# Kernel tuning notes

Measured on AMD Instinct MI355X. Metric: run time of the kernel, lower is better.

The kernel has to match this reference:

```python
import jax, jax.numpy as jnp
from jax import lax
import numpy as np

RADIUS = 2.0
K = 32          # max_neighbors
KNN = 3         # knn_num for FP interpolation
DEPTH = 3
NH = 16         # nhidden
NIN = 16
NOUT = 2
N = 16384
BOX = 32.0


def sqdist(a, b):
    # a: [M,3], b: [N,3] -> [M,N] squared distances (no [M,N,3] intermediate)
    d2 = (jnp.sum(a * a, -1)[:, None] + jnp.sum(b * b, -1)[None, :]
          - 2.0 * a @ b.T)
    return jnp.maximum(d2, 0.0)


def fps(pos, m):
    # farthest point sampling, deterministic start at index 0 (eval mode)
    n = pos.shape[0]
    def step(carry, _):
        mind, last = carry
        d = jnp.sum((pos - pos[last]) ** 2, axis=-1)
        mind = jnp.minimum(mind, d)
        nxt = jnp.argmax(mind).astype(jnp.int32)
        return (mind, nxt), nxt
    init = (jnp.full((n,), jnp.inf, dtype=pos.dtype), jnp.array(0, jnp.int32))
    _, rest = lax.scan(step, init, None, length=m - 1)
    return jnp.concatenate([jnp.zeros((1,), jnp.int32), rest])


def radius_group(pos_tgt, pos_src, r, k):
    # up-to-k neighbors of each target within radius r (nearest-first)
    d2 = sqdist(pos_tgt, pos_src)                      # [M,N]
    neg = jnp.where(d2 <= r * r, -d2, -jnp.inf)
    vals, cols = lax.top_k(neg, k)                     # [M,K]
    valid = jnp.isfinite(vals)
    return cols, valid


def knn_interpolate(x_c, pos_c, pos_f, k):
    d2 = sqdist(pos_f, pos_c)                          # [Nf, Nc]
    negv, nn = lax.top_k(-d2, k)                       # k nearest coarse pts
    w = 1.0 / jnp.maximum(-negv, 1e-16)
    w = w / jnp.sum(w, -1, keepdims=True)
    return jnp.sum(x_c[nn] * w[..., None], axis=1)     # [Nf, C]


def mlp2(h, W0, b0, W1, b1, act_last=True):
    h = jax.nn.relu(h @ W0 + b0)
    h = h @ W1 + b1
    return jax.nn.relu(h) if act_last else h


def setup_inputs() -> dict:
    key = jax.random.key(0)
    ks = jax.random.split(key, 24)
    s = 0.2
    dim_sa = NH + 3   # 19: PointConv concat(x_j, rel_pos)
    dim_fp = NH + NH  # 32: FP concat(interp, skip)
    return {
        "x": jax.random.normal(ks[0], (N, NIN), jnp.float32),
        "pos": jax.random.uniform(ks[1], (N, 3), jnp.float32) * BOX,
        "batch": jnp.zeros((N,), jnp.int32),
        "lin_in_W0": jax.random.normal(ks[2], (NIN, NH)) * s,
        "lin_in_b0": jnp.zeros((NH,), jnp.float32),
        "lin_in_W1": jax.random.normal(ks[3], (NH, NH)) * s,
        "lin_in_b1": jnp.zeros((NH,), jnp.float32),
        "sa_W0": jax.random.normal(ks[4], (DEPTH, dim_sa, dim_sa)) * s,
        "sa_b0": jnp.zeros((DEPTH, dim_sa), jnp.float32),
        "sa_W1": jax.random.normal(ks[5], (DEPTH, dim_sa, NH)) * s,
        "sa_b1": jnp.zeros((DEPTH, NH), jnp.float32),
        "fp_W0": jax.random.normal(ks[6], (DEPTH, dim_fp, dim_fp)) * s,
        "fp_b0": jnp.zeros((DEPTH, dim_fp), jnp.float32),
        "fp_W1": jax.random.normal(ks[7], (DEPTH, dim_fp, NH)) * s,
        "fp_b1": jnp.zeros((DEPTH, NH), jnp.float32),
        "lo_W0": jax.random.normal(ks[8], (NH, NH)) * s,
        "lo_b0": jnp.zeros((NH,), jnp.float32),
        "lo_W1": jax.random.normal(ks[9], (NH, NOUT)) * s,
        "lo_b1": jnp.zeros((NOUT,), jnp.float32),
    }


def reference(x, pos, batch,
              lin_in_W0, lin_in_b0, lin_in_W1, lin_in_b1,
              sa_W0, sa_b0, sa_W1, sa_b1,
              fp_W0, fp_b0, fp_W1, fp_b1,
              lo_W0, lo_b0, lo_W1, lo_b1):
    # lin_in MLP
    h = mlp2(x, lin_in_W0, lin_in_b0, lin_in_W1, lin_in_b1)
    sa = [(h, pos)]
    # SA (downsampling) path
    for i in range(DEPTH):
        xi, pi = sa[i]
        m = pi.shape[0] // 2                      # ratio = 0.5
        idx = fps(pi, m)
        pt = pi[idx]                              # sampled centers [M,3]
        cols, valid = radius_group(pt, pi, RADIUS, K)   # [M,K]
        xj = xi[cols]                             # [M,K,NH]
        rel = pi[cols] - pt[:, None, :]           # [M,K,3]
        msg = jnp.concatenate([xj, rel], -1)      # [M,K,19]
        msg = mlp2(msg, sa_W0[i], sa_b0[i], sa_W1[i], sa_b1[i])
        msg = jnp.where(valid[..., None], msg, -1e30)
        xn = jnp.max(msg, axis=1)                 # max aggregation (PointConv)
        sa.append((xn, pt))
    # FP (upsampling) path
    xf, pf = sa[DEPTH]
    for i in range(DEPTH - 1, -1, -1):
        xs, ps = sa[i]
        xi = knn_interpolate(xf, pf, ps, KNN)
        hcat = jnp.concatenate([xi, xs], -1)      # [Nf, 32]
        xf = mlp2(hcat, fp_W0[i], fp_b0[i], fp_W1[i], fp_b1[i])
        pf = ps
    # lin_out: relu then linear (act=['relu', None])
    return mlp2(xf, lo_W0, lo_b0, lo_W1, lo_b1, act_last=False)
```

## Files before the change

kernel.cpp:

```cpp
#include <hip/hip_runtime.h>
#include <stdint.h>


#define DEV static __device__ __forceinline__

DEV float fadd_(float a, float b){ return __fadd_rn(a,b); }
DEV float fsub_(float a, float b){ return __fsub_rn(a,b); }
DEV float fmul_(float a, float b){ return __fmul_rn(a,b); }
DEV float fdiv_(float a, float b){ return __fdiv_rn(a,b); }

DEV float dot3(float ax,float ay,float az,float bx,float by,float bz){
  return fmaf(az,bz, fmaf(ay,by, __fmul_rn(ax,bx)));
}
DEV float sqd(float na, float nb, float d){
  float t = __fadd_rn(na, nb);
  float u = __fmul_rn(2.0f, d);
  return fmaxf(__fsub_rn(t, u), 0.0f);
}

DEV float bbd2(float sx,float sy,float sz,
               float lx,float ly,float lz,float hx,float hy,float hz){
  float dx = fmaxf(fmaxf(fsub_(lx,sx), fsub_(sx,hx)), 0.0f);
  float dy = fmaxf(fmaxf(fsub_(ly,sy), fsub_(sy,hy)), 0.0f);
  float dz = fmaxf(fmaxf(fsub_(lz,sz), fsub_(sz,hz)), 0.0f);
  return fadd_(fadd_(fmul_(dx,dx),fmul_(dy,dy)),fmul_(dz,dz));
}

#define DPP0(src, ctrl, rm, bc) \
  __builtin_amdgcn_update_dpp(0, (int)(src), (ctrl), (rm), 0xf, (bc))

#define DPP64(dst, src, ctrl, rm, bc) { \
  uint32_t lo_ = (uint32_t)DPP0((uint32_t)(src), ctrl, rm, bc); \
  uint32_t hi_ = (uint32_t)DPP0((uint32_t)((src)>>32), ctrl, rm, bc); \
  (dst) = (((unsigned long long)hi_)<<32) | lo_; }

#define MERGE2(A1, A2, ctrl, rm, bc) { \
  unsigned long long b1_, b2_, mn_, mx_; \
  DPP64(b1_, A1, ctrl, rm, bc); \
  DPP64(b2_, A2, ctrl, rm, bc); \
  mn_ = (A1) < b1_ ? (A1) : b1_; \
  mx_ = (A2) > b2_ ? (A2) : b2_; \
  (A1) = (A1) > b1_ ? (A1) : b1_; \
  (A2) = mn_ > mx_ ? mn_ : mx_; }

DEV unsigned long long rdlane64(unsigned long long v, int l){
  uint32_t lo=(uint32_t)__builtin_amdgcn_readlane((int)(uint32_t)v, l);
  uint32_t hi=(uint32_t)__builtin_amdgcn_readlane((int)(uint32_t)(v>>32), l);
  return (((unsigned long long)hi)<<32)|lo;
}

DEV void wtop2(unsigned long long &A1, unsigned long long &A2){
  MERGE2(A1,A2,0x111,0xf,true)
  MERGE2(A1,A2,0x112,0xf,true)
  MERGE2(A1,A2,0x114,0xf,true)
  MERGE2(A1,A2,0x118,0xf,true)
  MERGE2(A1,A2,0x142,0xa,false)
  MERGE2(A1,A2,0x143,0xc,false)
  A1 = rdlane64(A1,63); A2 = rdlane64(A2,63);
}
DEV void htop2(unsigned long long &A1, unsigned long long &A2){
  MERGE2(A1,A2,0x111,0xf,true)
  MERGE2(A1,A2,0x112,0xf,true)
  MERGE2(A1,A2,0x114,0xf,true)
  MERGE2(A1,A2,0x118,0xf,true)
  MERGE2(A1,A2,0x142,0xa,false)
  A1 = rdlane64(A1,31); A2 = rdlane64(A2,31);
}

__global__ __launch_bounds__(256) void k_prep(
    const float* __restrict__ x, const float* __restrict__ pos,
    const float* __restrict__ W0, const float* __restrict__ b0,
    const float* __restrict__ W1, const float* __restrict__ b1,
    float4* __restrict__ pos4, float* __restrict__ h_out, int n)
{
  __shared__ float sW0[256], sb0[16], sW1[256], sb1[16];
  int tid = threadIdx.x;
  sW0[tid] = W0[tid];
  sW1[tid] = W1[tid];
  if (tid < 16){ sb0[tid] = b0[tid]; sb1[tid] = b1[tid]; }
  __syncthreads();
  int p = blockIdx.x*256 + tid;
  if (p >= n) return;

  float px = pos[3*p], py = pos[3*p+1], pz = pos[3*p+2];
  float nrm = fadd_(fadd_(fmul_(px,px), fmul_(py,py)), fmul_(pz,pz));
  pos4[p] = make_float4(px,py,pz,nrm);

  const float4* xr = (const float4*)(x + (size_t)p*16);
  float4 v0 = xr[0], v1 = xr[1], v2 = xr[2], v3 = xr[3];
  float xin[16] = {v0.x,v0.y,v0.z,v0.w, v1.x,v1.y,v1.z,v1.w,
                   v2.x,v2.y,v2.z,v2.w, v3.x,v3.y,v3.z,v3.w};
  float h1[16];
  #pragma unroll
  for (int o=0;o<16;o++){
    float acc = fmul_(xin[0], sW0[o]);
    #pragma unroll
    for (int k=1;k<16;k++) acc = fmaf(xin[k], sW0[k*16+o], acc);
    h1[o] = fmaxf(fadd_(acc, sb0[o]), 0.0f);
  }
  float h2[16];
  #pragma unroll
  for (int o=0;o<16;o++){
    float acc = fmul_(h1[0], sW1[o]);
    #pragma unroll
    for (int k=1;k<16;k++) acc = fmaf(h1[k], sW1[k*16+o], acc);
    h2[o] = fmaxf(fadd_(acc, sb1[o]), 0.0f);
  }
  float4* hw = (float4*)(h_out + (size_t)p*16);
  hw[0] = make_float4(h2[0], h2[1], h2[2], h2[3]);
  hw[1] = make_float4(h2[4], h2[5], h2[6], h2[7]);
  hw[2] = make_float4(h2[8], h2[9], h2[10],h2[11]);
  hw[3] = make_float4(h2[12],h2[13],h2[14],h2[15]);
}

DEV uint32_t expand4(uint32_t v){
  return (v&1u) | ((v&2u)<<2) | ((v&4u)<<4) | ((v&8u)<<6);
}
DEV int cellc(float v){
  int c = (int)(v*0.5f);
  return c < 0 ? 0 : (c > 15 ? 15 : c);
}
DEV uint32_t mkey(float4 p){
  return expand4((uint32_t)cellc(p.x))
       | (expand4((uint32_t)cellc(p.y))<<1)
       | (expand4((uint32_t)cellc(p.z))<<2);
}

__global__ __launch_bounds__(1024) void k_sort(
  const float4* __restrict__ nat, float4* __restrict__ srt,
  int* __restrict__ rank0, int n)
{
  __shared__ uint32_t hist[4096];
  __shared__ uint32_t gsum[1024];
  int tid = threadIdx.x;
  for (int i=tid;i<4096;i+=1024) hist[i]=0u;
  __syncthreads();
  for (int i=tid;i<n;i+=1024){
    float4 p = nat[i];
    atomicAdd(&hist[mkey(p)], 1u);
  }
  __syncthreads();
  uint32_t h0=hist[4*tid],h1=hist[4*tid+1],h2=hist[4*tid+2],h3=hist[4*tid+3];
  gsum[tid] = h0+h1+h2+h3;
  __syncthreads();
  for (int off=1; off<1024; off<<=1){
    uint32_t v = gsum[tid];
    uint32_t a = (tid>=off)? gsum[tid-off] : 0u;
    __syncthreads();
    gsum[tid] = v + a;
    __syncthreads();
  }
  uint32_t excl = (tid>0)? gsum[tid-1] : 0u;
  hist[4*tid]   = excl;
  hist[4*tid+1] = excl + h0;
  hist[4*tid+2] = excl + h0 + h1;
  hist[4*tid+3] = excl + h0 + h1 + h2;
  __syncthreads();
  for (int i=tid;i<n;i+=1024){
    float4 p = nat[i];
    uint32_t r = atomicAdd(&hist[mkey(p)], 1u);
    srt[r] = make_float4(p.x, p.y, p.z, __uint_as_float((uint32_t)i));
    if (i==0) *rank0 = (int)r;
  }
}

template<int P>
__global__ __attribute__((amdgpu_waves_per_eu(4,4)))
__launch_bounds__(1024) void k_fps5(
    const float4* __restrict__ sp4,
    const int* __restrict__ rank0p,
    float4* __restrict__ samp,
    int m)
{
  __shared__ float smind[P*1024];
  __shared__ uint32_t xch[2][32*5];
  const int t = threadIdx.x;
  const int lane = t & 63;
  const int w = t >> 6;

  float px[P], py[P], pz[P];
  uint32_t klo[P];
  float blox,bloy,bloz,bhix,bhiy,bhiz;
  #pragma unroll
  for (int k=0;k<P;k++){
    float4 p = sp4[t*P+k];
    px[k]=p.x; py[k]=p.y; pz[k]=p.z;
    uint32_t nat = __float_as_uint(p.w);
    klo[k] = ((0x3FFFu - nat)<<16) | (uint32_t)(t*P+k);
    smind[k*1024+t] = __builtin_inff();
    if (k==0){ blox=bhix=p.x; bloy=bhiy=p.y; bloz=bhiz=p.z; }
    else {
      blox=fminf(blox,p.x); bhix=fmaxf(bhix,p.x);
      bloy=fminf(bloy,p.y); bhiy=fmaxf(bhiy,p.y);
      bloz=fminf(bloz,p.z); bhiz=fmaxf(bhiz,p.z);
    }
  }

  float c1x,c1y,c1z, c2x=0.f,c2y=0.f,c2z=0.f;
  {
    int r0 = *rank0p;
    float4 s0 = sp4[r0];
    c1x=s0.x; c1y=s0.y; c1z=s0.z;
    if (t==0){
      float nr = fadd_(fadd_(fmul_(s0.x,s0.x),fmul_(s0.y,s0.y)),fmul_(s0.z,s0.z));
      samp[0] = make_float4(s0.x,s0.y,s0.z,nr);
    }
  }
  __syncthreads();

  unsigned long long tc1 = ((unsigned long long)0x7f800000u)<<32, tc2 = 0ull;
  bool own1 = false, own2 = false;
  uint32_t c1lo=0,c1hi=0, c2lo=0,c2hi=0;
  float o1x=0,o1y=0,o1z=0, o2x=0,o2y=0,o2z=0;

  int u2 = 0, sel = 1, round = 0;

  while (true){
    bool updp;
    {
      float cv = __uint_as_float((uint32_t)(tc1>>32));
      float dm = bbd2(c1x,c1y,c1z, blox,bloy,bloz,bhix,bhiy,bhiz);
      if (u2){
        float dd = bbd2(c2x,c2y,c2z, blox,bloy,bloz,bhix,bhiy,bhiz);
        dm = fminf(dm, dd);
      }
      updp = (fmul_(dm, 0.99999f) < cv);
    }
    if (__ballot(updp) != 0ull){
      if (updp){
        tc1 = 0ull; tc2 = 0ull;
        #pragma unroll
        for (int k=0;k<P;k++){
          float dx=fsub_(px[k],c1x), dy=fsub_(py[k],c1y), dz=fsub_(pz[k],c1z);
          float da = fadd_(fadd_(fmul_(dx,dx),fmul_(dy,dy)),fmul_(dz,dz));
          float nm = fminf(smind[k*1024+t], da);
          if (u2){
            float ex=fsub_(px[k],c2x), ey=fsub_(py[k],c2y), ez=fsub_(pz[k],c2z);
            float db = fadd_(fadd_(fmul_(ex,ex),fmul_(ey,ey)),fmul_(ez,ez));
            nm = fminf(nm, db);
          }
          smind[k*1024+t] = nm;
          unsigned long long key =
            (((unsigned long long)__float_as_uint(nm))<<32) | klo[k];
          bool g1 = key > tc1;
          unsigned long long nt2 = g1 ? tc1 : (key > tc2 ? key : tc2);
          tc1 = g1 ? key : tc1;
          tc2 = nt2;
        }
      }
      unsigned long long a1 = tc1, a2 = tc2;
      wtop2(a1, a2);
      own1 = (tc1 == a1);
      own2 = (tc1 == a2) || (tc2 == a2);
      int kk1 = (int)(a1 & (unsigned long long)(P-1));
      int kk2 = (int)(a2 & (unsigned long long)(P-1));
      float sx1=px[0], sy1=py[0], sz1=pz[0];
      float sx2=px[0], sy2=py[0], sz2=pz[0];
      #pragma unroll
      for (int j=1;j<P;j++){
        bool e1=(j==kk1), e2=(j==kk2);
        sx1=e1?px[j]:sx1; sy1=e1?py[j]:sy1; sz1=e1?pz[j]:sz1;
        sx2=e2?px[j]:sx2; sy2=e2?py[j]:sy2; sz2=e2?pz[j]:sz2;
      }
      c1lo=(uint32_t)a1; c1hi=(uint32_t)(a1>>32); o1x=sx1; o1y=sy1; o1z=sz1;
      c2lo=(uint32_t)a2; c2hi=(uint32_t)(a2>>32); o2x=sx2; o2y=sy2; o2z=sz2;
    }
    int par = round & 1;
    if (own1){
      int b = (w*2)*5;
      xch[par][b]=c1lo; xch[par][b+1]=c1hi;
      xch[par][b+2]=__float_as_uint(o1x);
      xch[par][b+3]=__float_as_uint(o1y);
      xch[par][b+4]=__float_as_uint(o1z);
    }
    if (own2){
      int b = (w*2+1)*5;
      xch[par][b]=c2lo; xch[par][b+1]=c2hi;
      xch[par][b+2]=__float_as_uint(o2x);
      xch[par][b+3]=__float_as_uint(o2y);
      xch[par][b+4]=__float_as_uint(o2z);
    }
    __syncthreads();
    unsigned long long cnd = 0ull;
    if (lane < 32){
      uint32_t lo = xch[par][lane*5], hi = xch[par][lane*5+1];
      cnd = (((unsigned long long)hi)<<32) | lo;
    }
    unsigned long long a1 = cnd, a2 = 0ull;
    htop2(a1, a2);
    unsigned long long b1 = __ballot(lane<32 && cnd==a1);
    unsigned long long b2 = __ballot(lane<32 && cnd==a2);
    int s1 = __ffsll(b1)-1;
    int s2 = __ffsll(b2)-1;
    float p1x=__uint_as_float(xch[par][s1*5+2]);
    float p1y=__uint_as_float(xch[par][s1*5+3]);
    float p1z=__uint_as_float(xch[par][s1*5+4]);
    float p2x=__uint_as_float(xch[par][s2*5+2]);
    float p2y=__uint_as_float(xch[par][s2*5+3]);
    float p2z=__uint_as_float(xch[par][s2*5+4]);
    float v2 = __uint_as_float((uint32_t)(a2>>32));
    float qx=fsub_(p2x,p1x), qy=fsub_(p2y,p1y), qz=fsub_(p2z,p1z);
    float q  = fadd_(fadd_(fmul_(qx,qx),fmul_(qy,qy)),fmul_(qz,qz));
    bool acc2 = (sel+1 < m) && (q >= v2);
    if (t==0){
      float nr = fadd_(fadd_(fmul_(p1x,p1x),fmul_(p1y,p1y)),fmul_(p1z,p1z));
      samp[sel] = make_float4(p1x,p1y,p1z,nr);
    }
    if (acc2 && t==1){
      float nr = fadd_(fadd_(fmul_(p2x,p2x),fmul_(p2y,p2y)),fmul_(p2z,p2z));
      samp[sel+1] = make_float4(p2x,p2y,p2z,nr);
    }
    sel += acc2 ? 2 : 1;
    round++;
    if (sel >= m) break;
    c1x=p1x; c1y=p1y; c1z=p1z;
    u2 = acc2 ? 1 : 0;
    if (acc2){ c2x=p2x; c2y=p2y; c2z=p2z; }
  }
}

#define SA_CAP 96

__global__ __launch_bounds__(256) void k_sa(
  const float4* __restrict__ spos, int n_src,
  const float4* __restrict__ tpos,
  const float*  __restrict__ F,
  const float* __restrict__ W0, const float* __restrict__ b0,
  const float* __restrict__ W1, const float* __restrict__ b1,
  float* __restrict__ Fout)
{
  __shared__ float sW0[361], sb0[19], sW1[304], sb1[16];
  __shared__ int   nidx[4][SA_CAP];
  __shared__ float nd2[4][SA_CAP];
  int tid = threadIdx.x;
  for (int i=tid;i<361;i+=256) sW0[i]=W0[i];
  for (int i=tid;i<304;i+=256) sW1[i]=W1[i];
  if (tid<19) sb0[tid]=b0[tid];
  if (tid<16) sb1[tid]=b1[tid];
  __syncthreads();

  int wv = tid >> 6, lane = tid & 63;
  int tg = blockIdx.x*4 + wv;
  float4 tp = tpos[tg];

  int cnt = 0;
  for (int base=0; base<n_src; base+=64){
    int j = base + lane;
    float4 sp = spos[j];
    float d2 = sqd(tp.w, sp.w, dot3(tp.x,tp.y,tp.z, sp.x,sp.y,sp.z));
    bool in = (d2 <= 4.0f);
    unsigned long long mk = __ballot(in);
    int pos = cnt + __popcll(mk & ((1ull<<lane)-1ull));
    if (in && pos < SA_CAP){ nidx[wv][pos]=j; nd2[wv][pos]=d2; }
    cnt += __popcll(mk);
  }
  if (cnt > SA_CAP) cnt = SA_CAP;

  if (cnt > 32){
    uint64_t tk0=0, tk1=0;
    for (int r=0;r<32;r++){
      float bvv = 3.5e38f; int bii = 0x7fffffff; int be = 0;
      for (int e=0;e<cnt;e++){
        bool done = (e<64) ? ((tk0>>e)&1ull) : ((tk1>>(e-64))&1ull);
        if (done) continue;
        float dv = nd2[wv][e]; int di = nidx[wv][e];
        if (dv < bvv || (dv == bvv && di < bii)){ bvv=dv; bii=di; be=e; }
      }
      if (be < 64) tk0 |= (1ull<<be); else tk1 |= (1ull<<(be-64));
    }
    int myi = 0; float myd = 0.0f;
    if (lane < 32){
      int seen = 0, sel = -1;
      for (int e=0;e<cnt && sel<0;e++){
        bool s = (e<64) ? ((tk0>>e)&1ull) : ((tk1>>(e-64))&1ull);
        if (s){ if (seen == lane) sel = e; seen++; }
      }
      myi = nidx[wv][sel]; myd = nd2[wv][sel];
    }
    __builtin_amdgcn_wave_barrier();
    if (lane < 32){ nidx[wv][lane]=myi; nd2[wv][lane]=myd; }
    __builtin_amdgcn_wave_barrier();
    cnt = 32;
  }

  float in19[19];
  #pragma unroll
  for (int k=0;k<19;k++) in19[k] = 0.0f;
  if (lane < cnt){
    int j = nidx[wv][lane];
    const float4* fr = (const float4*)(F + (size_t)j*16);
    float4 a=fr[0], b=fr[1], c=fr[2], d=fr[3];
    in19[0]=a.x; in19[1]=a.y; in19[2]=a.z; in19[3]=a.w;
    in19[4]=b.x; in19[5]=b.y; in19[6]=b.z; in19[7]=b.w;
    in19[8]=c.x; in19[9]=c.y; in19[10]=c.z; in19[11]=c.w;
    in19[12]=d.x; in19[13]=d.y; in19[14]=d.z; in19[15]=d.w;
    float4 sp = spos[j];
    in19[16]=fsub_(sp.x,tp.x); in19[17]=fsub_(sp.y,tp.y); in19[18]=fsub_(sp.z,tp.z);
  }
  float h[19];
  #pragma unroll
  for (int o=0;o<19;o++){
    float acc = fmul_(in19[0], sW0[o]);
    #pragma unroll
    for (int k=1;k<19;k++) acc = fmaf(in19[k], sW0[k*19+o], acc);
    h[o] = fmaxf(fadd_(acc, sb0[o]), 0.0f);
  }
  float outv[16];
  #pragma unroll
  for (int o=0;o<16;o++){
    float acc = fmul_(h[0], sW1[o]);
    #pragma unroll
    for (int k=1;k<19;k++) acc = fmaf(h[k], sW1[k*16+o], acc);
    float v = fmaxf(fadd_(acc, sb1[o]), 0.0f);
    outv[o] = (lane < cnt) ? v : -1e30f;
  }
  #pragma unroll
  for (int o=0;o<16;o++){
    float v = outv[o];
    #pragma unroll
    for (int s=1;s<64;s<<=1) v = fmaxf(v, __shfl_xor(v, s));
    outv[o] = v;
  }
  if (lane == 0){
    float4* dst = (float4*)(Fout + (size_t)tg*16);
    dst[0] = make_float4(outv[0], outv[1], outv[2], outv[3]);
    dst[1] = make_float4(outv[4], outv[5], outv[6], outv[7]);
    dst[2] = make_float4(outv[8], outv[9], outv[10],outv[11]);
    dst[3] = make_float4(outv[12],outv[13],outv[14],outv[15]);
  }
}

__global__ __launch_bounds__(256) void k_fp(
  const float4* __restrict__ fpos,
  const float4* __restrict__ cpos, int n_coarse,
  const float* __restrict__ Fc, const float* __restrict__ Fs,
  const float* __restrict__ W0, const float* __restrict__ b0,
  const float* __restrict__ W1, const float* __restrict__ b1,
  const float* __restrict__ loW0, const float* __restrict__ lob0,
  const float* __restrict__ loW1, const float* __restrict__ lob1,
  float* __restrict__ outp, int final_)
{
  __shared__ float sW0[1024], sb0[32], sW1[512], sb1[16];
  __shared__ float sLW0[256], sLb0[16], sLW1[32], sLb1[2];
  int tid = threadIdx.x;
  for (int i=tid;i<1024;i+=256) sW0[i]=W0[i];
  for (int i=tid;i<512;i+=256)  sW1[i]=W1[i];
  if (tid<32) sb0[tid]=b0[tid];
  if (tid<16) sb1[tid]=b1[tid];
  if (final_){
    sLW0[tid & 255] = loW0[tid & 255];
    if (tid<16) sLb0[tid]=lob0[tid];
    if (tid<32) sLW1[tid]=loW1[tid];
    if (tid<2)  sLb1[tid]=lob1[tid];
  }
  __syncthreads();

  int wv = tid >> 6, lane = tid & 63;
  int f = blockIdx.x*4 + wv;
  float4 fp = fpos[f];

  float c0v=3.5e38f, c1v=3.5e38f, c2v=3.5e38f;
  int   c0i=0x7fffffff, c1i=0x7fffffff, c2i=0x7fffffff;
  for (int j=lane; j<n_coarse; j+=64){
    float4 cp = cpos[j];
    float d2 = sqd(fp.w, cp.w, dot3(fp.x,fp.y,fp.z, cp.x,cp.y,cp.z));
    if (d2 < c2v || (d2 == c2v && j < c2i)){
      bool a0 = (d2 < c0v) || (d2 == c0v && j < c0i);
      bool a1 = (d2 < c1v) || (d2 == c1v && j < c1i);
      c2v = a1 ? c1v : d2;               c2i = a1 ? c1i : j;
      c1v = a0 ? c0v : (a1 ? d2 : c1v);  c1i = a0 ? c0i : (a1 ? j : c1i);
      c0v = a0 ? d2 : c0v;               c0i = a0 ? j  : c0i;
    }
  }
  float nnd[3]; int nni[3];
  #pragma unroll
  for (int r=0;r<3;r++){
    float v = c0v; int idx = c0i;
    #pragma unroll
    for (int s=1;s<64;s<<=1){
      float ov = __shfl_xor(v, s);
      int   oi = __shfl_xor(idx, s);
      bool tk = (ov < v) || (ov == v && oi < idx);
      v = tk ? ov : v; idx = tk ? oi : idx;
    }
    nnd[r] = v; nni[r] = idx;
    if (c0v == v && c0i == idx){
      c0v=c1v; c0i=c1i; c1v=c2v; c1i=c2i; c2v=3.5e38f; c2i=0x7fffffff;
    }
  }
  float w0 = fdiv_(1.0f, fmaxf(nnd[0], 1e-16f));
  float w1 = fdiv_(1.0f, fmaxf(nnd[1], 1e-16f));
  float w2 = fdiv_(1.0f, fmaxf(nnd[2], 1e-16f));
  float ws = fadd_(fadd_(w0,w1),w2);
  w0 = fdiv_(w0,ws); w1 = fdiv_(w1,ws); w2 = fdiv_(w2,ws);

  float hv = 0.0f;
  if (lane < 16){
    int c = lane;
    float x0 = Fc[(size_t)nni[0]*16 + c];
    float x1 = Fc[(size_t)nni[1]*16 + c];
    float x2 = Fc[(size_t)nni[2]*16 + c];
    hv = fadd_(fadd_(fmul_(w0,x0), fmul_(w1,x1)), fmul_(w2,x2));
  } else if (lane < 32){
    hv = Fs[(size_t)f*16 + (lane-16)];
  }
  int o1 = lane & 31;
  float acc = fmul_(__shfl(hv, 0), sW0[o1]);
  #pragma unroll
  for (int k=1;k<32;k++) acc = fmaf(__shfl(hv, k), sW0[k*32+o1], acc);
  float g1 = fmaxf(fadd_(acc, sb0[o1]), 0.0f);
  int o2 = lane & 15;
  float a2 = fmul_(__shfl(g1, 0), sW1[o2]);
  #pragma unroll
  for (int k=1;k<32;k++) a2 = fmaf(__shfl(g1, k), sW1[k*16+o2], a2);
  float g2 = fmaxf(fadd_(a2, sb1[o2]), 0.0f);

  if (!final_){
    if (lane < 16) outp[(size_t)f*16 + lane] = g2;
  } else {
    float a3 = fmul_(__shfl(g2, 0), sLW0[o2]);
    #pragma unroll
    for (int k=1;k<16;k++) a3 = fmaf(__shfl(g2, k), sLW0[k*16+o2], a3);
    float q = fmaxf(fadd_(a3, sLb0[o2]), 0.0f);
    int o3 = lane & 1;
    float a4 = fmul_(__shfl(q, 0), sLW1[o3]);
    #pragma unroll
    for (int k=1;k<16;k++) a4 = fmaf(__shfl(q, k), sLW1[k*2+o3], a4);
    a4 = fadd_(a4, sLb1[o3]);
    if (lane < 2) outp[(size_t)f*2 + lane] = a4;
  }
}

extern "C" void kernel_launch(void* const* d_in, const int* in_sizes, int n_in,
                              void* d_out, int out_size, void* d_ws, size_t ws_size,
                              hipStream_t stream) {
  (void)in_sizes; (void)n_in; (void)out_size; (void)ws_size;
  const float* x     = (const float*)d_in[0];
  const float* pos   = (const float*)d_in[1];
  const float* liW0  = (const float*)d_in[3];
  const float* lib0  = (const float*)d_in[4];
  const float* liW1  = (const float*)d_in[5];
  const float* lib1  = (const float*)d_in[6];
  const float* saW0  = (const float*)d_in[7];
  const float* sab0  = (const float*)d_in[8];
  const float* saW1  = (const float*)d_in[9];
  const float* sab1  = (const float*)d_in[10];
  const float* fpW0  = (const float*)d_in[11];
  const float* fpb0  = (const float*)d_in[12];
  const float* fpW1  = (const float*)d_in[13];
  const float* fpb1  = (const float*)d_in[14];
  const float* loW0  = (const float*)d_in[15];
  const float* lob0  = (const float*)d_in[16];
  const float* loW1  = (const float*)d_in[17];
  const float* lob1  = (const float*)d_in[18];
  float* out = (float*)d_out;

  char* ws = (char*)d_ws;
  size_t off = 0;
  auto alloc = [&](size_t bytes)->void* {
    void* p = ws + off;
    off += (bytes + 255) & ~(size_t)255;
    return p;
  };
  float4* P0 = (float4*)alloc(16384u*16);
  float4* P1 = (float4*)alloc(8192u*16);
  float4* P2 = (float4*)alloc(4096u*16);
  float4* P3 = (float4*)alloc(2048u*16);
  float*  F0 = (float*)alloc(16384u*16*4);
  float*  F1 = (float*)alloc(8192u*16*4);
  float*  F2 = (float*)alloc(4096u*16*4);
  float*  F3 = (float*)alloc(2048u*16*4);
  float*  G2 = (float*)alloc(4096u*16*4);
  float*  G1 = (float*)alloc(8192u*16*4);
  float4* S0 = (float4*)alloc(16384u*16);
  float4* S1 = (float4*)alloc(8192u*16);
  float4* S2 = (float4*)alloc(4096u*16);
  int*    R0 = (int*)alloc(256);

  k_prep<<<64,256,0,stream>>>(x,pos, liW0,lib0,liW1,lib1, P0,F0, 16384);

  k_sort<<<1,1024,0,stream>>>(P0, S0, R0+0, 16384);
  k_fps5<16><<<1,1024,0,stream>>>(S0, R0+0, P1, 8192);
  k_sa<<<2048,256,0,stream>>>(P0,16384, P1, F0, saW0,      sab0,    saW1,      sab1,    F1);
  k_sort<<<1,1024,0,stream>>>(P1, S1, R0+1, 8192);
  k_fps5<8><<<1,1024,0,stream>>>(S1, R0+1, P2, 4096);
  k_sa<<<1024,256,0,stream>>>(P1, 8192, P2, F1, saW0+361,  sab0+19, saW1+304,  sab1+16, F2);
  k_sort<<<1,1024,0,stream>>>(P2, S2, R0+2, 4096);
  k_fps5<4><<<1,1024,0,stream>>>(S2, R0+2, P3, 2048);
  k_sa<<< 512,256,0,stream>>>(P2, 4096, P3, F2, saW0+722,  sab0+38, saW1+608,  sab1+32, F3);

  k_fp<<<1024,256,0,stream>>>(P2, P3,2048, F3, F2,
      fpW0+2048, fpb0+64, fpW1+1024, fpb1+32,
      loW0,lob0,loW1,lob1, G2, 0);
  k_fp<<<2048,256,0,stream>>>(P1, P2,4096, G2, F1,
      fpW0+1024, fpb0+32, fpW1+512,  fpb1+16,
      loW0,lob0,loW1,lob1, G1, 0);
  k_fp<<<4096,256,0,stream>>>(P0, P1,8192, G1, F0,
      fpW0,      fpb0,    fpW1,      fpb1,
      loW0,lob0,loW1,lob1, out, 1);
}
```

Baseline: 20.61 ms.

## Extend FPS speculative selection from top-2 to top-4 candidates per round

The farthest-point-sampling kernel now keeps a per-thread and per-wave top-4 instead of top-2, and accepts up to four new samples per round when each candidate is at least as far from the earlier accepted candidates as its own min-distance. This cuts the number of serial block-wide rounds and barriers in the single-block FPS loop. Candidate coordinates are now re-read from global memory by sorted index instead of being passed through shared memory. In exchange each round does more DPP merge work and more distance updates per point.

```diff
diff --git a/kernel.cpp b/kernel.cpp
--- a/kernel.cpp
+++ b/kernel.cpp
@@ -16,6 +16,14 @@
   float t = __fadd_rn(na, nb);
   float u = __fmul_rn(2.0f, d);
   return fmaxf(__fsub_rn(t, u), 0.0f);
+}
+
+DEV float d2f_(float ax,float ay,float az,float bx,float by,float bz){
+  float dx=fsub_(ax,bx), dy=fsub_(ay,by), dz=fsub_(az,bz);
+  return fadd_(fadd_(fmul_(dx,dx),fmul_(dy,dy)),fmul_(dz,dz));
+}
+DEV float nrm3_(float x,float y,float z){
+  return fadd_(fadd_(fmul_(x,x),fmul_(y,y)),fmul_(z,z));
 }
 
 DEV float bbd2(float sx,float sy,float sz,
@@ -26,6 +34,10 @@
   return fadd_(fadd_(fmul_(dx,dx),fmul_(dy,dy)),fmul_(dz,dz));
 }
 
+DEV float rfl_f(float v){
+  return __int_as_float(__builtin_amdgcn_readfirstlane(__float_as_int(v)));
+}
+
 #define DPP0(src, ctrl, rm, bc) \
   __builtin_amdgcn_update_dpp(0, (int)(src), (ctrl), (rm), 0xf, (bc))
 
@@ -34,14 +46,21 @@
   uint32_t hi_ = (uint32_t)DPP0((uint32_t)((src)>>32), ctrl, rm, bc); \
   (dst) = (((unsigned long long)hi_)<<32) | lo_; }
 
-#define MERGE2(A1, A2, ctrl, rm, bc) { \
-  unsigned long long b1_, b2_, mn_, mx_; \
+#define MERGE4(A1,A2,A3,A4, ctrl, rm, bc) { \
+  unsigned long long b1_,b2_,b3_,b4_, m1_,m2_,m3_,m4_, t_; \
   DPP64(b1_, A1, ctrl, rm, bc); \
   DPP64(b2_, A2, ctrl, rm, bc); \
-  mn_ = (A1) < b1_ ? (A1) : b1_; \
-  mx_ = (A2) > b2_ ? (A2) : b2_; \
-  (A1) = (A1) > b1_ ? (A1) : b1_; \
-  (A2) = mn_ > mx_ ? mn_ : mx_; }
+  DPP64(b3_, A3, ctrl, rm, bc); \
+  DPP64(b4_, A4, ctrl, rm, bc); \
+  m1_ = (A1) > b4_ ? (A1) : b4_; \
+  m2_ = (A2) > b3_ ? (A2) : b3_; \
+  m3_ = (A3) > b2_ ? (A3) : b2_; \
+  m4_ = (A4) > b1_ ? (A4) : b1_; \
+  t_ = m1_ < m3_ ? m1_ : m3_;  m1_ = m1_ > m3_ ? m1_ : m3_;  m3_ = t_; \
+  t_ = m2_ < m4_ ? m2_ : m4_;  m2_ = m2_ > m4_ ? m2_ : m4_;  m4_ = t_; \
+  t_ = m1_ < m2_ ? m1_ : m2_;  m1_ = m1_ > m2_ ? m1_ : m2_;  m2_ = t_; \
+  t_ = m3_ < m4_ ? m3_ : m4_;  m3_ = m3_ > m4_ ? m3_ : m4_;  m4_ = t_; \
+  (A1)=m1_; (A2)=m2_; (A3)=m3_; (A4)=m4_; }
 
 DEV unsigned long long rdlane64(unsigned long long v, int l){
   uint32_t lo=(uint32_t)__builtin_amdgcn_readlane((int)(uint32_t)v, l);
@@ -49,22 +68,16 @@
   return (((unsigned long long)hi)<<32)|lo;
 }
 
-DEV void wtop2(unsigned long long &A1, unsigned long long &A2){
-  MERGE2(A1,A2,0x111,0xf,true)
-  MERGE2(A1,A2,0x112,0xf,true)
-  MERGE2(A1,A2,0x114,0xf,true)
-  MERGE2(A1,A2,0x118,0xf,true)
-  MERGE2(A1,A2,0x142,0xa,false)
-  MERGE2(A1,A2,0x143,0xc,false)
+DEV void wtop4(unsigned long long &A1, unsigned long long &A2,
+               unsigned long long &A3, unsigned long long &A4){
+  MERGE4(A1,A2,A3,A4,0x111,0xf,true)
+  MERGE4(A1,A2,A3,A4,0x112,0xf,true)
+  MERGE4(A1,A2,A3,A4,0x114,0xf,true)
+  MERGE4(A1,A2,A3,A4,0x118,0xf,true)
+  MERGE4(A1,A2,A3,A4,0x142,0xa,false)
+  MERGE4(A1,A2,A3,A4,0x143,0xc,false)
   A1 = rdlane64(A1,63); A2 = rdlane64(A2,63);
-}
-DEV void htop2(unsigned long long &A1, unsigned long long &A2){
-  MERGE2(A1,A2,0x111,0xf,true)
-  MERGE2(A1,A2,0x112,0xf,true)
-  MERGE2(A1,A2,0x114,0xf,true)
-  MERGE2(A1,A2,0x118,0xf,true)
-  MERGE2(A1,A2,0x142,0xa,false)
-  A1 = rdlane64(A1,31); A2 = rdlane64(A2,31);
+  A3 = rdlane64(A3,63); A4 = rdlane64(A4,63);
 }
 
 __global__ __launch_bounds__(256) void k_prep(
@@ -166,14 +179,14 @@
 
 template<int P>
 __global__ __attribute__((amdgpu_waves_per_eu(4,4)))
-__launch_bounds__(1024) void k_fps5(
+__launch_bounds__(1024) void k_fps6(
     const float4* __restrict__ sp4,
     const int* __restrict__ rank0p,
     float4* __restrict__ samp,
     int m)
 {
   __shared__ float smind[P*1024];
-  __shared__ uint32_t xch[2][32*5];
+  __shared__ unsigned long long xch[2][64];
   const int t = threadIdx.x;
   const int lane = t & 63;
   const int w = t >> 6;
@@ -196,126 +209,98 @@
     }
   }
 
-  float c1x,c1y,c1z, c2x=0.f,c2y=0.f,c2z=0.f;
+  float c0x,c0y,c0z;
+  float c1x=0.f,c1y=0.f,c1z=0.f, c2x=0.f,c2y=0.f,c2z=0.f;
+  float c3x=0.f,c3y=0.f,c3z=0.f;
   {
     int r0 = *rank0p;
     float4 s0 = sp4[r0];
-    c1x=s0.x; c1y=s0.y; c1z=s0.z;
+    c0x=s0.x; c0y=s0.y; c0z=s0.z;
     if (t==0){
-      float nr = fadd_(fadd_(fmul_(s0.x,s0.x),fmul_(s0.y,s0.y)),fmul_(s0.z,s0.z));
-      samp[0] = make_float4(s0.x,s0.y,s0.z,nr);
-    }
-  }
-  __syncthreads();
-
-  unsigned long long tc1 = ((unsigned long long)0x7f800000u)<<32, tc2 = 0ull;
-  bool own1 = false, own2 = false;
-  uint32_t c1lo=0,c1hi=0, c2lo=0,c2hi=0;
-  float o1x=0,o1y=0,o1z=0, o2x=0,o2y=0,o2z=0;
-
-  int u2 = 0, sel = 1, round = 0;
+      samp[0] = make_float4(s0.x,s0.y,s0.z, nrm3_(s0.x,s0.y,s0.z));
+    }
+  }
+  __syncthreads();
+
+  unsigned long long tc1 = ((unsigned long long)0x7f800000u)<<32;
+  unsigned long long tc2 = 0ull, tc3 = 0ull, tc4 = 0ull;
+  unsigned long long a1=0ull,a2=0ull,a3=0ull,a4=0ull;
+
+  int u = 1, sel = 1, round = 0;
 
   while (true){
     bool updp;
     {
       float cv = __uint_as_float((uint32_t)(tc1>>32));
-      float dm = bbd2(c1x,c1y,c1z, blox,bloy,bloz,bhix,bhiy,bhiz);
-      if (u2){
-        float dd = bbd2(c2x,c2y,c2z, blox,bloy,bloz,bhix,bhiy,bhiz);
-        dm = fminf(dm, dd);
-      }
+      float dm = bbd2(c0x,c0y,c0z, blox,bloy,bloz,bhix,bhiy,bhiz);
+      if (u>1) dm = fminf(dm, bbd2(c1x,c1y,c1z, blox,bloy,bloz,bhix,bhiy,bhiz));
+      if (u>2) dm = fminf(dm, bbd2(c2x,c2y,c2z, blox,bloy,bloz,bhix,bhiy,bhiz));
+      if (u>3) dm = fminf(dm, bbd2(c3x,c3y,c3z, blox,bloy,bloz,bhix,bhiy,bhiz));
       updp = (fmul_(dm, 0.99999f) < cv);
     }
     if (__ballot(updp) != 0ull){
       if (updp){
-        tc1 = 0ull; tc2 = 0ull;
+        tc1 = 0ull; tc2 = 0ull; tc3 = 0ull; tc4 = 0ull;
         #pragma unroll
         for (int k=0;k<P;k++){
-          float dx=fsub_(px[k],c1x), dy=fsub_(py[k],c1y), dz=fsub_(pz[k],c1z);
-          float da = fadd_(fadd_(fmul_(dx,dx),fmul_(dy,dy)),fmul_(dz,dz));
-          float nm = fminf(smind[k*1024+t], da);
-          if (u2){
-            float ex=fsub_(px[k],c2x), ey=fsub_(py[k],c2y), ez=fsub_(pz[k],c2z);
-            float db = fadd_(fadd_(fmul_(ex,ex),fmul_(ey,ey)),fmul_(ez,ez));
-            nm = fminf(nm, db);
-          }
+          float nm = smind[k*1024+t];
+          nm = fminf(nm, d2f_(px[k],py[k],pz[k], c0x,c0y,c0z));
+          if (u>1) nm = fminf(nm, d2f_(px[k],py[k],pz[k], c1x,c1y,c1z));
+          if (u>2) nm = fminf(nm, d2f_(px[k],py[k],pz[k], c2x,c2y,c2z));
+          if (u>3) nm = fminf(nm, d2f_(px[k],py[k],pz[k], c3x,c3y,c3z));
           smind[k*1024+t] = nm;
           unsigned long long key =
             (((unsigned long long)__float_as_uint(nm))<<32) | klo[k];
-          bool g1 = key > tc1;
-          unsigned long long nt2 = g1 ? tc1 : (key > tc2 ? key : tc2);
-          tc1 = g1 ? key : tc1;
-          tc2 = nt2;
+          bool g1_ = key > tc1;
+          bool g2_ = key > tc2;
+          bool g3_ = key > tc3;
+          bool g4_ = key > tc4;
+          tc4 = g4_ ? (g3_ ? tc3 : key) : tc4;
+          tc3 = g3_ ? (g2_ ? tc2 : key) : tc3;
+          tc2 = g2_ ? (g1_ ? tc1 : key) : tc2;
+          tc1 = g1_ ? key : tc1;
         }
       }
-      unsigned long long a1 = tc1, a2 = tc2;
-      wtop2(a1, a2);
-      own1 = (tc1 == a1);
-      own2 = (tc1 == a2) || (tc2 == a2);
-      int kk1 = (int)(a1 & (unsigned long long)(P-1));
-      int kk2 = (int)(a2 & (unsigned long long)(P-1));
-      float sx1=px[0], sy1=py[0], sz1=pz[0];
-      float sx2=px[0], sy2=py[0], sz2=pz[0];
-      #pragma unroll
-      for (int j=1;j<P;j++){
-        bool e1=(j==kk1), e2=(j==kk2);
-        sx1=e1?px[j]:sx1; sy1=e1?py[j]:sy1; sz1=e1?pz[j]:sz1;
-        sx2=e2?px[j]:sx2; sy2=e2?py[j]:sy2; sz2=e2?pz[j]:sz2;
-      }
-      c1lo=(uint32_t)a1; c1hi=(uint32_t)(a1>>32); o1x=sx1; o1y=sy1; o1z=sz1;
-      c2lo=(uint32_t)a2; c2hi=(uint32_t)(a2>>32); o2x=sx2; o2y=sy2; o2z=sz2;
+      a1=tc1; a2=tc2; a3=tc3; a4=tc4;
+      wtop4(a1,a2,a3,a4);
     }
     int par = round & 1;
-    if (own1){
-      int b = (w*2)*5;
-      xch[par][b]=c1lo; xch[par][b+1]=c1hi;
-      xch[par][b+2]=__float_as_uint(o1x);
-      xch[par][b+3]=__float_as_uint(o1y);
-      xch[par][b+4]=__float_as_uint(o1z);
-    }
-    if (own2){
-      int b = (w*2+1)*5;
-      xch[par][b]=c2lo; xch[par][b+1]=c2hi;
-      xch[par][b+2]=__float_as_uint(o2x);
-      xch[par][b+3]=__float_as_uint(o2y);
-      xch[par][b+4]=__float_as_uint(o2z);
+    if (lane < 4){
+      unsigned long long pv = (lane==0)?a1:((lane==1)?a2:((lane==2)?a3:a4));
+      xch[par][w*4+lane] = pv;
     }
     __syncthreads();
-    unsigned long long cnd = 0ull;
-    if (lane < 32){
-      uint32_t lo = xch[par][lane*5], hi = xch[par][lane*5+1];
-      cnd = (((unsigned long long)hi)<<32) | lo;
-    }
-    unsigned long long a1 = cnd, a2 = 0ull;
-    htop2(a1, a2);
-    unsigned long long b1 = __ballot(lane<32 && cnd==a1);
-    unsigned long long b2 = __ballot(lane<32 && cnd==a2);
-    int s1 = __ffsll(b1)-1;
-    int s2 = __ffsll(b2)-1;
-    float p1x=__uint_as_float(xch[par][s1*5+2]);
-    float p1y=__uint_as_float(xch[par][s1*5+3]);
-    float p1z=__uint_as_float(xch[par][s1*5+4]);
-    float p2x=__uint_as_float(xch[par][s2*5+2]);
-    float p2y=__uint_as_float(xch[par][s2*5+3]);
-    float p2z=__uint_as_float(xch[par][s2*5+4]);
-    float v2 = __uint_as_float((uint32_t)(a2>>32));
-    float qx=fsub_(p2x,p1x), qy=fsub_(p2y,p1y), qz=fsub_(p2z,p1z);
-    float q  = fadd_(fadd_(fmul_(qx,qx),fmul_(qy,qy)),fmul_(qz,qz));
-    bool acc2 = (sel+1 < m) && (q >= v2);
-    if (t==0){
-      float nr = fadd_(fadd_(fmul_(p1x,p1x),fmul_(p1y,p1y)),fmul_(p1z,p1z));
-      samp[sel] = make_float4(p1x,p1y,p1z,nr);
-    }
-    if (acc2 && t==1){
-      float nr = fadd_(fadd_(fmul_(p2x,p2x),fmul_(p2y,p2y)),fmul_(p2z,p2z));
-      samp[sel+1] = make_float4(p2x,p2y,p2z,nr);
-    }
-    sel += acc2 ? 2 : 1;
-    round++;
+    unsigned long long g1v = xch[par][lane];
+    unsigned long long g2v = 0ull, g3v = 0ull, g4v = 0ull;
+    wtop4(g1v,g2v,g3v,g4v);
+    float4 f1 = sp4[(int)(g1v & 0xFFFFull)];
+    float4 f2 = sp4[(int)(g2v & 0xFFFFull)];
+    float4 f3 = sp4[(int)(g3v & 0xFFFFull)];
+    float4 f4 = sp4[(int)(g4v & 0xFFFFull)];
+    float v2 = __uint_as_float((uint32_t)(g2v>>32));
+    float v3 = __uint_as_float((uint32_t)(g3v>>32));
+    float v4 = __uint_as_float((uint32_t)(g4v>>32));
+    float q12 = d2f_(f2.x,f2.y,f2.z, f1.x,f1.y,f1.z);
+    bool acc2 = (sel+1 < m) && (q12 >= v2);
+    float q13 = d2f_(f3.x,f3.y,f3.z, f1.x,f1.y,f1.z);
+    float q23 = d2f_(f3.x,f3.y,f3.z, f2.x,f2.y,f2.z);
+    bool acc3 = acc2 && (sel+2 < m) && (fminf(q13,q23) >= v3);
+    float q14 = d2f_(f4.x,f4.y,f4.z, f1.x,f1.y,f1.z);
+    float q24 = d2f_(f4.x,f4.y,f4.z, f2.x,f2.y,f2.z);
+    float q34 = d2f_(f4.x,f4.y,f4.z, f3.x,f3.y,f3.z);
+    bool acc4 = acc3 && (sel+3 < m) && (fminf(fminf(q14,q24),q34) >= v4);
+    if (t==0)          samp[sel  ] = make_float4(f1.x,f1.y,f1.z, nrm3_(f1.x,f1.y,f1.z));
+    if (acc2 && t==1)  samp[sel+1] = make_float4(f2.x,f2.y,f2.z, nrm3_(f2.x,f2.y,f2.z));
+    if (acc3 && t==2)  samp[sel+2] = make_float4(f3.x,f3.y,f3.z, nrm3_(f3.x,f3.y,f3.z));
+    if (acc4 && t==3)  samp[sel+3] = make_float4(f4.x,f4.y,f4.z, nrm3_(f4.x,f4.y,f4.z));
+    int nacc = 1 + (acc2?1:0) + (acc3?1:0) + (acc4?1:0);
+    sel += nacc; round++;
     if (sel >= m) break;
-    c1x=p1x; c1y=p1y; c1z=p1z;
-    u2 = acc2 ? 1 : 0;
-    if (acc2){ c2x=p2x; c2y=p2y; c2z=p2z; }
+    u   = __builtin_amdgcn_readfirstlane(nacc);
+    c0x = rfl_f(f1.x); c0y = rfl_f(f1.y); c0z = rfl_f(f1.z);
+    c1x = rfl_f(f2.x); c1y = rfl_f(f2.y); c1z = rfl_f(f2.z);
+    c2x = rfl_f(f3.x); c2y = rfl_f(f3.y); c2z = rfl_f(f3.z);
+    c3x = rfl_f(f4.x); c3y = rfl_f(f4.y); c3z = rfl_f(f4.z);
   }
 }
 
@@ -580,13 +565,13 @@
   k_prep<<<64,256,0,stream>>>(x,pos, liW0,lib0,liW1,lib1, P0,F0, 16384);
 
   k_sort<<<1,1024,0,stream>>>(P0, S0, R0+0, 16384);
-  k_fps5<16><<<1,1024,0,stream>>>(S0, R0+0, P1, 8192);
+  k_fps6<16><<<1,1024,0,stream>>>(S0, R0+0, P1, 8192);
   k_sa<<<2048,256,0,stream>>>(P0,16384, P1, F0, saW0,      sab0,    saW1,      sab1,    F1);
   k_sort<<<1,1024,0,stream>>>(P1, S1, R0+1, 8192);
-  k_fps5<8><<<1,1024,0,stream>>>(S1, R0+1, P2, 4096);
+  k_fps6<8><<<1,1024,0,stream>>>(S1, R0+1, P2, 4096);
   k_sa<<<1024,256,0,stream>>>(P1, 8192, P2, F1, saW0+361,  sab0+19, saW1+304,  sab1+16, F2);
   k_sort<<<1,1024,0,stream>>>(P2, S2, R0+2, 4096);
-  k_fps5<4><<<1,1024,0,stream>>>(S2, R0+2, P3, 2048);
+  k_fps6<4><<<1,1024,0,stream>>>(S2, R0+2, P3, 2048);
   k_sa<<< 512,256,0,stream>>>(P2, 4096, P3, F2, saW0+722,  sab0+38, saW1+608,  sab1+32, F3);
 
   k_fp<<<1024,256,0,stream>>>(P2, P3,2048, F3, F2,
```

Result: slower. 24.95 ms (+21.0%).

## Select up to four FPS points per round using top-4 and mutual-distance acceptance

Applied to the files above, without the earlier changes.

Adds a new FPS kernel for the first level that finds the top four candidates per round through a DPP-based top-4 merge. It then accepts candidates 2-4 only when they stay farther from the earlier picks than their own min-distance, which preserves the sequential FPS order. This is meant to cut the number of serial block-wide rounds and __syncthreads barriers in the latency-bound single-block FPS loop. In exchange, each round does more reduction work and carries more register pressure, and the exact tie and float equivalence to sequential FPS depends on the acceptance test.

```diff
diff --git a/kernel.cpp b/kernel.cpp
--- a/kernel.cpp
+++ b/kernel.cpp
@@ -16,6 +16,14 @@
   float t = __fadd_rn(na, nb);
   float u = __fmul_rn(2.0f, d);
   return fmaxf(__fsub_rn(t, u), 0.0f);
+}
+
+DEV float d2f_(float ax,float ay,float az,float bx,float by,float bz){
+  float dx=fsub_(ax,bx), dy=fsub_(ay,by), dz=fsub_(az,bz);
+  return fadd_(fadd_(fmul_(dx,dx),fmul_(dy,dy)),fmul_(dz,dz));
+}
+DEV float nrm3_(float x,float y,float z){
+  return fadd_(fadd_(fmul_(x,x),fmul_(y,y)),fmul_(z,z));
 }
 
 DEV float bbd2(float sx,float sy,float sz,
@@ -24,6 +32,10 @@
   float dy = fmaxf(fmaxf(fsub_(ly,sy), fsub_(sy,hy)), 0.0f);
   float dz = fmaxf(fmaxf(fsub_(lz,sz), fsub_(sz,hz)), 0.0f);
   return fadd_(fadd_(fmul_(dx,dx),fmul_(dy,dy)),fmul_(dz,dz));
+}
+
+DEV float rfl_f(float v){
+  return __int_as_float(__builtin_amdgcn_readfirstlane(__float_as_int(v)));
 }
 
 #define DPP0(src, ctrl, rm, bc) \
@@ -43,6 +55,22 @@
   (A1) = (A1) > b1_ ? (A1) : b1_; \
   (A2) = mn_ > mx_ ? mn_ : mx_; }
 
+#define MERGE4(A1,A2,A3,A4, ctrl, rm, bc) { \
+  unsigned long long b1_,b2_,b3_,b4_, m1_,m2_,m3_,m4_, t_; \
+  DPP64(b1_, A1, ctrl, rm, bc); \
+  DPP64(b2_, A2, ctrl, rm, bc); \
+  DPP64(b3_, A3, ctrl, rm, bc); \
+  DPP64(b4_, A4, ctrl, rm, bc); \
+  m1_ = (A1) > b4_ ? (A1) : b4_; \
+  m2_ = (A2) > b3_ ? (A2) : b3_; \
+  m3_ = (A3) > b2_ ? (A3) : b2_; \
+  m4_ = (A4) > b1_ ? (A4) : b1_; \
+  t_ = m1_ < m3_ ? m1_ : m3_;  m1_ = m1_ > m3_ ? m1_ : m3_;  m3_ = t_; \
+  t_ = m2_ < m4_ ? m2_ : m4_;  m2_ = m2_ > m4_ ? m2_ : m4_;  m4_ = t_; \
+  t_ = m1_ < m2_ ? m1_ : m2_;  m1_ = m1_ > m2_ ? m1_ : m2_;  m2_ = t_; \
+  t_ = m3_ < m4_ ? m3_ : m4_;  m3_ = m3_ > m4_ ? m3_ : m4_;  m4_ = t_; \
+  (A1)=m1_; (A2)=m2_; (A3)=m3_; (A4)=m4_; }
+
 DEV unsigned long long rdlane64(unsigned long long v, int l){
   uint32_t lo=(uint32_t)__builtin_amdgcn_readlane((int)(uint32_t)v, l);
   uint32_t hi=(uint32_t)__builtin_amdgcn_readlane((int)(uint32_t)(v>>32), l);
@@ -65,6 +93,28 @@
   MERGE2(A1,A2,0x118,0xf,true)
   MERGE2(A1,A2,0x142,0xa,false)
   A1 = rdlane64(A1,31); A2 = rdlane64(A2,31);
+}
+
+DEV void wtop4(unsigned long long &A1, unsigned long long &A2,
+               unsigned long long &A3, unsigned long long &A4){
+  MERGE4(A1,A2,A3,A4,0x111,0xf,true)
+  MERGE4(A1,A2,A3,A4,0x112,0xf,true)
+  MERGE4(A1,A2,A3,A4,0x114,0xf,true)
+  MERGE4(A1,A2,A3,A4,0x118,0xf,true)
+  MERGE4(A1,A2,A3,A4,0x142,0xa,false)
+  MERGE4(A1,A2,A3,A4,0x143,0xc,false)
+  A1 = rdlane64(A1,63); A2 = rdlane64(A2,63);
+  A3 = rdlane64(A3,63); A4 = rdlane64(A4,63);
+}
+
+DEV void qtop4(unsigned long long &A1, unsigned long long &A2,
+               unsigned long long &A3, unsigned long long &A4){
+  MERGE4(A1,A2,A3,A4,0x111,0xf,true)
+  MERGE4(A1,A2,A3,A4,0x112,0xf,true)
+  MERGE4(A1,A2,A3,A4,0x114,0xf,true)
+  MERGE4(A1,A2,A3,A4,0x118,0xf,true)
+  A1 = rdlane64(A1,15); A2 = rdlane64(A2,15);
+  A3 = rdlane64(A3,15); A4 = rdlane64(A4,15);
 }
 
 __global__ __launch_bounds__(256) void k_prep(
@@ -161,6 +211,152 @@
     uint32_t r = atomicAdd(&hist[mkey(p)], 1u);
     srt[r] = make_float4(p.x, p.y, p.z, __uint_as_float((uint32_t)i));
     if (i==0) *rank0 = (int)r;
+  }
+}
+
+template<int P>
+__global__ __attribute__((amdgpu_waves_per_eu(4,4)))
+__launch_bounds__(1024) void k_fps10(
+    const float4* __restrict__ sp4,
+    const int* __restrict__ rank0p,
+    float4* __restrict__ samp,
+    int m)
+{
+  __shared__ float smind[P*1024];
+  __shared__ __attribute__((aligned(16))) unsigned long long xch[2][64];
+  const int t = threadIdx.x;
+  const int lane = t & 63;
+  const int w = t >> 6;
+
+  float px[P], py[P], pz[P];
+  uint32_t klo[P];
+  float blox,bloy,bloz,bhix,bhiy,bhiz;
+  #pragma unroll
+  for (int k=0;k<P;k++){
+    float4 p = sp4[t*P+k];
+    px[k]=p.x; py[k]=p.y; pz[k]=p.z;
+    uint32_t nat = __float_as_uint(p.w);
+    klo[k] = ((0x3FFFu - nat)<<16) | (uint32_t)(t*P+k);
+    smind[k*1024+t] = __builtin_inff();
+    if (k==0){ blox=bhix=p.x; bloy=bhiy=p.y; bloz=bhiz=p.z; }
+    else {
+      blox=fminf(blox,p.x); bhix=fmaxf(bhix,p.x);
+      bloy=fminf(bloy,p.y); bhiy=fmaxf(bhiy,p.y);
+      bloz=fminf(bloz,p.z); bhiz=fmaxf(bhiz,p.z);
+    }
+  }
+
+  float c0x,c0y,c0z;
+  float c1x=0.f,c1y=0.f,c1z=0.f, c2x=0.f,c2y=0.f,c2z=0.f;
+  float c3x=0.f,c3y=0.f,c3z=0.f;
+  {
+    int r0 = *rank0p;
+    float4 s0 = sp4[r0];
+    c0x=s0.x; c0y=s0.y; c0z=s0.z;
+    if (t==0){
+      samp[0] = make_float4(s0.x,s0.y,s0.z, nrm3_(s0.x,s0.y,s0.z));
+    }
+  }
+  __syncthreads();
+
+  unsigned long long tc1 = ((unsigned long long)0x7f800000u)<<32;
+  unsigned long long tc2 = 0ull, tc3 = 0ull, tc4 = 0ull;
+  unsigned long long a1=0ull,a2=0ull,a3=0ull,a4=0ull;
+
+  int u = 1, sel = 1, round = 0;
+
+  while (true){
+    float cv = __uint_as_float((uint32_t)(tc1>>32));
+    bool act0, act1=false, act2=false, act3=false;
+    act0 = fmul_(bbd2(c0x,c0y,c0z, blox,bloy,bloz,bhix,bhiy,bhiz), 0.99999f) < cv;
+    if (u>1) act1 = fmul_(bbd2(c1x,c1y,c1z, blox,bloy,bloz,bhix,bhiy,bhiz), 0.99999f) < cv;
+    if (u>2) act2 = fmul_(bbd2(c2x,c2y,c2z, blox,bloy,bloz,bhix,bhiy,bhiz), 0.99999f) < cv;
+    if (u>3) act3 = fmul_(bbd2(c3x,c3y,c3z, blox,bloy,bloz,bhix,bhiy,bhiz), 0.99999f) < cv;
+    bool updp = act0 | act1 | act2 | act3;
+    if (__ballot(updp) != 0ull){
+      if (updp){
+        float nm[P];
+        #pragma unroll
+        for (int k=0;k<P;k++) nm[k] = smind[k*1024+t];
+        if (act0){
+          #pragma unroll
+          for (int k=0;k<P;k++)
+            nm[k] = fminf(nm[k], d2f_(px[k],py[k],pz[k], c0x,c0y,c0z));
+        }
+        if (u>1){ if (act1){
+          #pragma unroll
+          for (int k=0;k<P;k++)
+            nm[k] = fminf(nm[k], d2f_(px[k],py[k],pz[k], c1x,c1y,c1z));
+        }}
+        if (u>2){ if (act2){
+          #pragma unroll
+          for (int k=0;k<P;k++)
+            nm[k] = fminf(nm[k], d2f_(px[k],py[k],pz[k], c2x,c2y,c2z));
+        }}
+        if (u>3){ if (act3){
+          #pragma unroll
+          for (int k=0;k<P;k++)
+            nm[k] = fminf(nm[k], d2f_(px[k],py[k],pz[k], c3x,c3y,c3z));
+        }}
+        tc1 = 0ull; tc2 = 0ull; tc3 = 0ull; tc4 = 0ull;
+        #pragma unroll
+        for (int k=0;k<P;k++){
+          smind[k*1024+t] = nm[k];
+          unsigned long long key =
+            (((unsigned long long)__float_as_uint(nm[k]))<<32) | klo[k];
+          bool g1_ = key > tc1;
+          bool g2_ = key > tc2;
+          bool g3_ = key > tc3;
+          bool g4_ = key > tc4;
+          tc4 = g4_ ? (g3_ ? tc3 : key) : tc4;
+          tc3 = g3_ ? (g2_ ? tc2 : key) : tc3;
+          tc2 = g2_ ? (g1_ ? tc1 : key) : tc2;
+          tc1 = g1_ ? key : tc1;
+        }
+      }
+      a1=tc1; a2=tc2; a3=tc3; a4=tc4;
+      wtop4(a1,a2,a3,a4);
+    }
+    int par = round & 1;
+    if (lane < 4){
+      unsigned long long pv = (lane==0)?a1:((lane==1)?a2:((lane==2)?a3:a4));
+      xch[par][w*4+lane] = pv;
+    }
+    __syncthreads();
+    unsigned long long g1v=0ull, g2v=0ull, g3v=0ull, g4v=0ull;
+    if (lane < 16){
+      const unsigned long long* b = &xch[par][lane*4];
+      g1v=b[0]; g2v=b[1]; g3v=b[2]; g4v=b[3];
+    }
+    qtop4(g1v,g2v,g3v,g4v);
+    float4 f1 = sp4[(int)(g1v & 0xFFFFull)];
+    float4 f2 = sp4[(int)(g2v & 0xFFFFull)];
+    float4 f3 = sp4[(int)(g3v & 0xFFFFull)];
+    float4 f4 = sp4[(int)(g4v & 0xFFFFull)];
+    float v2 = __uint_as_float((uint32_t)(g2v>>32));
+    float v3 = __uint_as_float((uint32_t)(g3v>>32));
+    float v4 = __uint_as_float((uint32_t)(g4v>>32));
+    float q12 = d2f_(f2.x,f2.y,f2.z, f1.x,f1.y,f1.z);
+    bool acc2 = (sel+1 < m) && (q12 >= v2);
+    float q13 = d2f_(f3.x,f3.y,f3.z, f1.x,f1.y,f1.z);
+    float q23 = d2f_(f3.x,f3.y,f3.z, f2.x,f2.y,f2.z);
+    bool acc3 = acc2 && (sel+2 < m) && (fminf(q13,q23) >= v3);
+    float q14 = d2f_(f4.x,f4.y,f4.z, f1.x,f1.y,f1.z);
+    float q24 = d2f_(f4.x,f4.y,f4.z, f2.x,f2.y,f2.z);
+    float q34 = d2f_(f4.x,f4.y,f4.z, f3.x,f3.y,f3.z);
+    bool acc4 = acc3 && (sel+3 < m) && (fminf(fminf(q14,q24),q34) >= v4);
+    if (t==0)          samp[sel  ] = make_float4(f1.x,f1.y,f1.z, nrm3_(f1.x,f1.y,f1.z));
+    if (acc2 && t==1)  samp[sel+1] = make_float4(f2.x,f2.y,f2.z, nrm3_(f2.x,f2.y,f2.z));
+    if (acc3 && t==2)  samp[sel+2] = make_float4(f3.x,f3.y,f3.z, nrm3_(f3.x,f3.y,f3.z));
+    if (acc4 && t==3)  samp[sel+3] = make_float4(f4.x,f4.y,f4.z, nrm3_(f4.x,f4.y,f4.z));
+    int nacc = 1 + (acc2?1:0) + (acc3?1:0) + (acc4?1:0);
+    sel += nacc; round++;
+    if (sel >= m) break;
+    u   = __builtin_amdgcn_readfirstlane(nacc);
+    c0x = rfl_f(f1.x); c0y = rfl_f(f1.y); c0z = rfl_f(f1.z);
+    c1x = rfl_f(f2.x); c1y = rfl_f(f2.y); c1z = rfl_f(f2.z);
+    c2x = rfl_f(f3.x); c2y = rfl_f(f3.y); c2z = rfl_f(f3.z);
+    c3x = rfl_f(f4.x); c3y = rfl_f(f4.y); c3z = rfl_f(f4.z);
   }
 }
 
@@ -580,12 +776,12 @@
   k_prep<<<64,256,0,stream>>>(x,pos, liW0,lib0,liW1,lib1, P0,F0, 16384);
 
   k_sort<<<1,1024,0,stream>>>(P0, S0, R0+0, 16384);
-  k_fps5<16><<<1,1024,0,stream>>>(S0, R0+0, P1, 8192);
+  k_fps10<16><<<1,1024,0,stream>>>(S0, R0+0, P1, 8192);
   k_sa<<<2048,256,0,stream>>>(P0,16384, P1, F0, saW0,      sab0,    saW1,      sab1,    F1);
   k_sort<<<1,1024,0,stream>>>(P1, S1, R0+1, 8192);
   k_fps5<8><<<1,1024,0,stream>>>(S1, R0+1, P2, 4096);
   k_sa<<<1024,256,0,stream>>>(P1, 8192, P2, F1, saW0+361,  sab0+19, saW1+304,  sab1+16, F2);
-  k_sort<<<1,1024,0,stream>>>(P2, S2, R0+2, 4096);
+  k_sort<<<1,1024,0,stream>>>(P2, S2, R0+2, 2048? 4096 : 4096);
   k_fps5<4><<<1,1024,0,stream>>>(S2, R0+2, P3, 2048);
   k_sa<<< 512,256,0,stream>>>(P2, 4096, P3, F2, saW0+722,  sab0+38, saW1+608,  sab1+32, F3);
 
```

New measurement: 19.17 ms. 7.0% less time.
